# Performance work log

Hardware: AMD Instinct MI355X
Metric: run time of the kernel (lower is better)

The kernel has to match this reference:

```python
import jax, jax.numpy as jnp
import numpy as np

EMB = 128
EDGE = 32
STEPS = 3


def _lrelu(x):
    return jax.nn.leaky_relu(x, negative_slope=0.01)


def setup_inputs() -> dict:
    key = jax.random.key(0)
    ks = jax.random.split(key, 16)
    N, E, G = 50000, 400000, 256
    x = jax.random.normal(ks[0], (N, EMB), jnp.float32)
    edge_attr = jax.random.normal(ks[1], (E, EDGE), jnp.float32)
    edge_index = jax.random.randint(ks[2], (2, E), 0, N, jnp.int64)
    batch_ind = jnp.sort(jax.random.randint(ks[3], (N,), 0, G, jnp.int64))
    data_lens = jax.random.randint(ks[4], (G,), 0, G, jnp.int64)
    s = 1.0 / np.sqrt(EMB)
    Wm = jax.random.normal(ks[5], (STEPS, EMB + EDGE, EMB), jnp.float32) * s
    bm = jnp.zeros((STEPS, EMB), jnp.float32)
    Wa = jax.random.normal(ks[6], (STEPS, 3 * EMB, EMB), jnp.float32) * s
    ba = jnp.zeros((STEPS, EMB), jnp.float32)
    Wgate = jax.random.normal(ks[7], (STEPS, EMB), jnp.float32) * s
    bgate = jnp.zeros((STEPS,), jnp.float32)
    Wfeat = jax.random.normal(ks[8], (STEPS, EMB, EMB), jnp.float32) * s
    bfeat = jnp.zeros((STEPS, EMB), jnp.float32)
    Wt = jax.random.normal(ks[9], (STEPS, 2 * EMB, EMB), jnp.float32) * s
    bt = jnp.zeros((STEPS, EMB), jnp.float32)
    return {"x": x, "edge_attr": edge_attr, "Wm": Wm, "bm": bm, "Wa": Wa,
            "ba": ba, "Wgate": Wgate, "bgate": bgate, "Wfeat": Wfeat,
            "bfeat": bfeat, "Wt": Wt, "bt": bt, "edge_index": edge_index,
            "batch_ind": batch_ind, "num_graphs": 256, "data_lens": data_lens}


def reference(x, edge_attr, Wm, bm, Wa, ba, Wgate, bgate, Wfeat, bfeat, Wt, bt,
              edge_index, batch_ind, num_graphs, data_lens):
    N = x.shape[0]
    src, dst = edge_index[0], edge_index[1]  # PyG: x_j = x[src], aggregate at dst
    xg = jnp.zeros((num_graphs, EMB), x.dtype)  # xg_init is None -> zeros
    for s in range(STEPS):
        # GraphNet: gather -> message MLP -> scatter-max -> update MLP + residual
        xg_node = xg[batch_ind]                                   # [N, emb]
        z = jnp.concatenate([x[src], edge_attr], axis=1)          # [E, emb+edge]
        m = _lrelu(z @ Wm[s] + bm[s])                             # [E, emb]
        agg = jax.ops.segment_max(m, dst, num_segments=N)         # [N, emb]
        agg = jnp.where(jnp.isneginf(agg), 0.0, agg)              # PyG fills empty with 0
        z2 = jnp.concatenate([x, xg_node, agg], axis=1)           # [N, 3*emb]
        x = _lrelu(z2 @ Wa[s] + ba[s]) + x
        # GlobalNode: segment-softmax attention pooling + transform + residual
        gate = x @ Wgate[s] + bgate[s]                            # [N]
        gmax = jax.ops.segment_max(gate, batch_ind, num_segments=num_graphs)
        gmax = jnp.where(jnp.isneginf(gmax), 0.0, gmax)
        e = jnp.exp(gate - gmax[batch_ind])
        denom = jax.ops.segment_sum(e, batch_ind, num_segments=num_graphs)
        alpha = e / denom[batch_ind]                              # [N]
        feat = _lrelu(x @ Wfeat[s] + bfeat[s])                    # [N, emb]
        pooled = jax.ops.segment_sum(alpha[:, None] * feat, batch_ind,
                                     num_segments=num_graphs)     # [G, emb]
        cat = jnp.concatenate([pooled, xg], axis=1)               # [G, 2*emb]
        xg = _lrelu(cat @ Wt[s] + bt[s]) + xg
    return x, xg
```

## Files before the change

kernel.cpp:

```cpp
#include <hip/hip_runtime.h>
#include <hip/hip_bf16.h>

#define EMB 128
#define EDGE 32
#define STEPS 3

typedef short bf8s __attribute__((ext_vector_type(8)));
typedef float f32x4 __attribute__((ext_vector_type(4)));

__device__ __forceinline__ float lrelu(float v) { return v > 0.0f ? v : 0.01f * v; }
__device__ __forceinline__ unsigned short f2bf(float f) {
    unsigned u = __float_as_uint(f);
    u += 0x7fffu + ((u >> 16) & 1u);
    return (unsigned short)(u >> 16);
}
__device__ __forceinline__ float bf2f(unsigned short s) {
    return __uint_as_float(((unsigned)s) << 16);
}
__device__ __forceinline__ unsigned pk2bf(float x, float y) {
    __hip_bfloat162 h = __float22bfloat162_rn(make_float2(x, y));
    return *(unsigned*)&h;
}

__global__ void k_hist(const int* __restrict__ dst, int E, int* __restrict__ deg) {
    int e = blockIdx.x * 256 + threadIdx.x;
    if (e < E) atomicAdd(&deg[dst[e]], 1);
}

__global__ void k_scan1(const int* __restrict__ deg, int N, int* __restrict__ rowptr,
                        int* __restrict__ bsums) {
    __shared__ int s[256];
    int t = threadIdx.x;
    int i = blockIdx.x * 256 + t;
    int v = (i < N) ? deg[i] : 0;
    s[t] = v;
    __syncthreads();
#pragma unroll
    for (int off = 1; off < 256; off <<= 1) {
        int x = (t >= off) ? s[t - off] : 0;
        __syncthreads();
        s[t] += x;
        __syncthreads();
    }
    if (i < N) rowptr[i] = s[t] - v;
    if (t == 255) bsums[blockIdx.x] = s[255];
}

__global__ void k_scan2(int* __restrict__ bsums, int NB) {
    __shared__ int s[256];
    __shared__ int carry;
    int t = threadIdx.x;
    if (t == 0) carry = 0;
    __syncthreads();
    for (int base = 0; base < NB; base += 256) {
        int i = base + t;
        int v = (i < NB) ? bsums[i] : 0;
        s[t] = v;
        __syncthreads();
#pragma unroll
        for (int off = 1; off < 256; off <<= 1) {
            int x = (t >= off) ? s[t - off] : 0;
            __syncthreads();
            s[t] += x;
            __syncthreads();
        }
        int excl = s[t] - v + carry;
        if (i < NB) bsums[i] = excl;
        int tot = s[255];
        __syncthreads();
        if (t == 0) carry += tot;
        __syncthreads();
    }
}

__global__ void k_scan3(int* __restrict__ rowptr, const int* __restrict__ bsums,
                        int* __restrict__ cursor, int N, int E) {
    int i = blockIdx.x * 256 + threadIdx.x;
    if (i < N) {
        int v = rowptr[i] + bsums[i >> 8];
        rowptr[i] = v;
        cursor[i] = v;
    }
    if (i == 0) rowptr[N] = E;
}

__global__ void k_fill(const int* __restrict__ src, const int* __restrict__ dst, int E,
                       int* __restrict__ cursor, int2* __restrict__ sp2) {
    int e = blockIdx.x * 256 + threadIdx.x;
    if (e >= E) return;
    int d = dst[e];
    int p = atomicAdd(&cursor[d], 1);
    sp2[p] = make_int2(src[e], e);
}

__global__ __launch_bounds__(256) void k_eaperm(const float* __restrict__ ea,
                                                const int2* __restrict__ sp2,
                                                unsigned short* __restrict__ ea16p,
                                                int* __restrict__ srcp, int E) {
    int p = blockIdx.x * 256 + threadIdx.x;
    if (p >= E) return;
    int2 sp = sp2[p];
    srcp[p] = sp.x;
    const float4* er = (const float4*)(ea + (size_t)sp.y * EDGE);
    union { unsigned u[16]; int4 v[4]; } o;
#pragma unroll
    for (int q = 0; q < 8; ++q) {
        float4 v = er[q];
        o.u[2 * q]     = pk2bf(v.x, v.y);
        o.u[2 * q + 1] = pk2bf(v.z, v.w);
    }
    int4* dp = (int4*)(ea16p + (size_t)p * EDGE);
#pragma unroll
    for (int q = 0; q < 4; ++q) dp[q] = o.v[q];
}

__global__ __launch_bounds__(256) void k_setup(const float* __restrict__ x0,
                                               unsigned short* __restrict__ x16,
                                               int N, int XB, int NB,
                                               const float* __restrict__ ba,
                                               float* __restrict__ gb,
                                               float* __restrict__ xg_a,
                                               const int* __restrict__ batch,
                                               int* __restrict__ gstart, int G,
                                               unsigned short* __restrict__ h16,
                                               int* __restrict__ deg) {
    int b = blockIdx.x, t = threadIdx.x;
    if (b < XB) {
        size_t idx = ((size_t)b * 256 + t) * 8;
        if (idx < (size_t)N * EMB) {
            const float4* s = (const float4*)(x0 + idx);
            float4 v0 = s[0], v1 = s[1];
            union { bf8s v; unsigned u[4]; } o;
            o.u[0] = pk2bf(v0.x, v0.y);
            o.u[1] = pk2bf(v0.z, v0.w);
            o.u[2] = pk2bf(v1.x, v1.y);
            o.u[3] = pk2bf(v1.z, v1.w);
            *(bf8s*)(x16 + idx) = o.v;
        }
        return;
    }
    b -= XB;
    if (b < NB) {
        int i = b * 256 + t;
        if (i < N) deg[i] = 0;
        return;
    }
    b -= NB;
    if (b < G) {
        if (t < EMB) gb[(size_t)b * EMB + t] = ba[t];
        else xg_a[(size_t)b * EMB + (t - EMB)] = 0.f;
        if (t == 0) {
            int lo = 0, hi = N;
            while (lo < hi) {
                int mid = (lo + hi) >> 1;
                if (batch[mid] < b) lo = mid + 1; else hi = mid;
            }
            gstart[b] = lo;
        }
        return;
    }
    if (t < EMB) h16[(size_t)N * EMB + t] = 0xFF80u;
    if (t == EMB) gstart[G] = N;
}

__global__ __launch_bounds__(256) void k_wpack(const float* __restrict__ Wm,
                                               const float* __restrict__ Wa,
                                               const float* __restrict__ Wfeat,
                                               unsigned short* __restrict__ wpack) {
    int gid = blockIdx.x * 256 + threadIdx.x;
    int unit = gid >> 14;
    int e = gid & 16383;
    int s = unit / 5, u = unit % 5;
    const float* src; int rows;
    switch (u) {
        case 0: src = Wm + (size_t)s * 160 * EMB;             rows = 128; break;
        case 1: src = Wm + (size_t)s * 160 * EMB + 128 * EMB; rows = 32;  break;
        case 2: src = Wa + (size_t)s * 384 * EMB;             rows = 128; break;
        case 3: src = Wa + (size_t)s * 384 * EMB + 256 * EMB; rows = 128; break;
        default: src = Wfeat + (size_t)s * EMB * EMB;         rows = 128; break;
    }
    int k = e >> 7, n = e & 127;
    if (k >= rows) return;
    unsigned short b = f2bf(src[(size_t)k * EMB + n]);
    int kc = k >> 5, c = n >> 4, lane = (n & 15) | (((k & 31) >> 3) << 4), j = k & 7;
    wpack[(size_t)unit * 16384 + ((size_t)(kc * 8 + c) * 64 + lane) * 8 + j] = b;
}

__device__ __forceinline__ void loadAa(const unsigned short* __restrict__ A16, int row0,
                                       int wv, int lane, int N, bf8s af[4]) {
    int li = lane & 15, oct = lane >> 4;
    int m = row0 + wv * 16 + li;
    if (m >= N) m = N - 1;
    const bf8s* ar = (const bf8s*)(A16 + (size_t)m * EMB);
#pragma unroll
    for (int kc = 0; kc < 4; ++kc) af[kc] = ar[kc * 4 + oct];
}
__device__ __forceinline__ void stageB(const unsigned short* __restrict__ Bp,
                                       unsigned short* lB, int tid) {
#pragma unroll
    for (int i = 0; i < 8; ++i) {
        int idx = tid + i * 256;
        ((int4*)lB)[idx] = ((const int4*)Bp)[idx];
    }
}
__device__ __forceinline__ void mfma128r(const bf8s af[4], const unsigned short* lB,
                                         f32x4 acc[8], int lane) {
#pragma unroll
    for (int kc = 0; kc < 4; ++kc) {
#pragma unroll
        for (int c = 0; c < 8; ++c) {
            bf8s b = *(const bf8s*)&lB[((kc * 8 + c) * 64 + lane) * 8];
            acc[c] = __builtin_amdgcn_mfma_f32_16x16x32_bf16(af[kc], b, acc[c], 0, 0, 0);
        }
    }
}

__global__ __launch_bounds__(256) void k_gemm_bias(const unsigned short* __restrict__ A16,
                                                   const unsigned short* __restrict__ Bp,
                                                   const float* __restrict__ bias,
                                                   unsigned short* __restrict__ C, int N) {
    __shared__ unsigned short lB[16384];
    int tid = threadIdx.x, wv = tid >> 6, lane = tid & 63;
    int row0 = blockIdx.x * 64;
    stageB(Bp, lB, tid);
    bf8s af[4];
    loadAa(A16, row0, wv, lane, N, af);
    __syncthreads();
    f32x4 acc[8];
#pragma unroll
    for (int c = 0; c < 8; ++c) acc[c] = (f32x4){0.f, 0.f, 0.f, 0.f};
    mfma128r(af, lB, acc, lane);
    int li = lane & 15, quad = lane >> 4;
    float bcol[8];
#pragma unroll
    for (int c = 0; c < 8; ++c) bcol[c] = bias[c * 16 + li];
#pragma unroll
    for (int rr = 0; rr < 4; ++rr) {
        int m = row0 + wv * 16 + quad * 4 + rr;
        if (m < N) {
            union { bf8s v; unsigned u[4]; } o;
#pragma unroll
            for (int j = 0; j < 4; ++j)
                o.u[j] = pk2bf(acc[2 * j][rr] + bcol[2 * j],
                               acc[2 * j + 1][rr] + bcol[2 * j + 1]);
            *(bf8s*)&C[(size_t)m * EMB + li * 8] = o.v;
        }
    }
}

__global__ __launch_bounds__(256) void k_gemm_node(unsigned short* __restrict__ x16,
                                                   const unsigned short* __restrict__ agg16,
                                                   const unsigned short* __restrict__ BpX,
                                                   const unsigned short* __restrict__ BpA,
                                                   const float* __restrict__ gb,
                                                   const int* __restrict__ batch,
                                                   float* __restrict__ xout_f32,
                                                   const float* __restrict__ wg,
                                                   const float* __restrict__ bg,
                                                   float* __restrict__ gate, int N) {
    __shared__ unsigned short lB[16384];
    int tid = threadIdx.x, wv = tid >> 6, lane = tid & 63;
    int row0 = blockIdx.x * 64;
    stageB(BpX, lB, tid);
    bf8s af[4];
    loadAa(x16, row0, wv, lane, N, af);
    __syncthreads();
    f32x4 acc[8];
#pragma unroll
    for (int c = 0; c < 8; ++c) acc[c] = (f32x4){0.f, 0.f, 0.f, 0.f};
    mfma128r(af, lB, acc, lane);
    __syncthreads();
    stageB(BpA, lB, tid);
    loadAa(agg16, row0, wv, lane, N, af);
    __syncthreads();
    mfma128r(af, lB, acc, lane);
    int li = lane & 15, quad = lane >> 4;
    float gpart[4] = {0.f, 0.f, 0.f, 0.f};
#pragma unroll
    for (int c = 0; c < 8; ++c) {
        int col = c * 16 + li;
        float wgc = wg[col];
#pragma unroll
        for (int rr = 0; rr < 4; ++rr) {
            int m = row0 + wv * 16 + quad * 4 + rr;
            if (m < N) {
                int g = batch[m];
                float b = gb[(size_t)g * EMB + col];
                float res = bf2f(x16[(size_t)m * EMB + col]);
                float v = lrelu(acc[c][rr] + b) + res;
                x16[(size_t)m * EMB + col] = f2bf(v);
                if (xout_f32) xout_f32[(size_t)m * EMB + col] = v;
                gpart[rr] = fmaf(v, wgc, gpart[rr]);
            }
        }
    }
#pragma unroll
    for (int rr = 0; rr < 4; ++rr) {
#pragma unroll
        for (int off = 1; off < 16; off <<= 1)
            gpart[rr] += __shfl_xor(gpart[rr], off, 64);
    }
    if (li == 0) {
        float b0 = bg[0];
#pragma unroll
        for (int rr = 0; rr < 4; ++rr) {
            int m = row0 + wv * 16 + quad * 4 + rr;
            if (m < N) gate[m] = gpart[rr] + b0;
        }
    }
}

__global__ __launch_bounds__(256) void k_gemm_feat(const unsigned short* __restrict__ A16,
                                                   const unsigned short* __restrict__ Bp,
                                                   const float* __restrict__ bias,
                                                   const float* __restrict__ gate,
                                                   const float* __restrict__ gmax,
                                                   const float* __restrict__ denom,
                                                   const int* __restrict__ batch,
                                                   float* __restrict__ pooled, int N) {
    __shared__ unsigned short lB[16384];
    int tid = threadIdx.x, wv = tid >> 6, lane = tid & 63;
    int row0 = blockIdx.x * 64;
    stageB(Bp, lB, tid);
    bf8s af[4];
    loadAa(A16, row0, wv, lane, N, af);
    __syncthreads();
    f32x4 acc[8];
#pragma unroll
    for (int c = 0; c < 8; ++c) acc[c] = (f32x4){0.f, 0.f, 0.f, 0.f};
    mfma128r(af, lB, acc, lane);
    int li = lane & 15, quad = lane >> 4;
    int rb = row0 + wv * 16;
    if (rb >= N) return;
    float alpha[4];
    int grow[4];
#pragma unroll
    for (int rr = 0; rr < 4; ++rr) {
        int m = rb + quad * 4 + rr;
        if (m < N) {
            int g = batch[m];
            grow[rr] = g;
            alpha[rr] = __expf(gate[m] - gmax[g]) / denom[g];
        } else { alpha[rr] = 0.f; grow[rr] = 0; }
    }
    int gs = batch[rb];
    int mlast = rb + 15; if (mlast >= N) mlast = N - 1;
    bool uni = (gs == batch[mlast]);
#pragma unroll
    for (int c = 0; c < 8; ++c) {
        int col = c * 16 + li;
        float b = bias[col];
        float v0 = alpha[0] * lrelu(acc[c][0] + b);
        float v1 = alpha[1] * lrelu(acc[c][1] + b);
        float v2 = alpha[2] * lrelu(acc[c][2] + b);
        float v3 = alpha[3] * lrelu(acc[c][3] + b);
        if (uni) {
            float s = (v0 + v1) + (v2 + v3);
            s += __shfl_xor(s, 16, 64);
            s += __shfl_xor(s, 32, 64);
            if (quad == 0) atomicAdd(&pooled[(size_t)gs * EMB + col], s);
        } else {
            if (rb + quad * 4 + 0 < N) atomicAdd(&pooled[(size_t)grow[0] * EMB + col], v0);
            if (rb + quad * 4 + 1 < N) atomicAdd(&pooled[(size_t)grow[1] * EMB + col], v1);
            if (rb + quad * 4 + 2 < N) atomicAdd(&pooled[(size_t)grow[2] * EMB + col], v2);
            if (rb + quad * 4 + 3 < N) atomicAdd(&pooled[(size_t)grow[3] * EMB + col], v3);
        }
    }
}

__global__ __launch_bounds__(256) void k_gseg(const float* __restrict__ gate,
                                              const int* __restrict__ gstart,
                                              float* __restrict__ gmax,
                                              float* __restrict__ denom,
                                              float* __restrict__ pooled) {
    int g = blockIdx.x;
    int t = threadIdx.x;
    if (t < EMB) pooled[(size_t)g * EMB + t] = 0.f;
    int s0 = gstart[g], s1 = gstart[g + 1];
    __shared__ float red[256];
    float mx = -__builtin_inff();
    for (int i = s0 + t; i < s1; i += 256) mx = fmaxf(mx, gate[i]);
    red[t] = mx;
    __syncthreads();
#pragma unroll
    for (int off = 128; off; off >>= 1) {
        if (t < off) red[t] = fmaxf(red[t], red[t + off]);
        __syncthreads();
    }
    float m = red[0];
    __syncthreads();
    float sum = 0.f;
    for (int i = s0 + t; i < s1; i += 256) sum += __expf(gate[i] - m);
    red[t] = sum;
    __syncthreads();
#pragma unroll
    for (int off = 128; off; off >>= 1) {
        if (t < off) red[t] += red[t + off];
        __syncthreads();
    }
    if (t == 0) {
        gmax[g] = (s1 > s0) ? m : 0.f;
        denom[g] = red[0];
    }
}

__global__ __launch_bounds__(128) void k_xg(const float* __restrict__ pooled,
                                            const float* __restrict__ xg,
                                            const float* __restrict__ Wt,
                                            const float* __restrict__ bt,
                                            float* __restrict__ xg_out,
                                            const float* __restrict__ WaGn,
                                            const float* __restrict__ ban,
                                            float* __restrict__ gb) {
    int g = blockIdx.x, c = threadIdx.x;
    __shared__ float row[256];
    row[c] = pooled[(size_t)g * EMB + c];
    row[c + 128] = xg[(size_t)g * EMB + c];
    __syncthreads();
    float acc = bt[c];
#pragma unroll 8
    for (int k = 0; k < 256; ++k) acc = fmaf(row[k], Wt[(size_t)k * EMB + c], acc);
    float v = lrelu(acc) + row[c + 128];
    xg_out[(size_t)g * EMB + c] = v;
    if (WaGn) {
        __syncthreads();
        row[c] = v;
        __syncthreads();
        float a2 = ban[c];
#pragma unroll 8
        for (int k = 0; k < EMB; ++k) a2 = fmaf(row[k], WaGn[(size_t)k * EMB + c], a2);
        gb[(size_t)g * EMB + c] = a2;
    }
}

__global__ __launch_bounds__(256) void k_fagg(const unsigned short* __restrict__ h,
                                              const unsigned short* __restrict__ ea16p,
                                              const int* __restrict__ srcp,
                                              const int* __restrict__ rowptr,
                                              const unsigned short* __restrict__ Bp,
                                              unsigned short* __restrict__ agg, int N) {
    __shared__ unsigned short lB[4096];
    int tid = threadIdx.x;
    ((int4*)lB)[tid]       = ((const int4*)Bp)[tid];
    ((int4*)lB)[tid + 256] = ((const int4*)Bp)[tid + 256];
    __syncthreads();
    int wv = tid >> 6, lane = tid & 63;
    int li = lane & 15, oct = lane >> 4;
    int nA = blockIdx.x * 8 + wv * 2;
    if (nA >= N) return;
    int nB = nA + 1;
    bool hasB = (nB < N);
    int r0 = rowptr[nA];
    int r1 = rowptr[nA + 1];
    int r2 = hasB ? rowptr[nB + 1] : r1;
    int degA = r1 - r0, degB = r2 - r1;

    float vmA[8], vmB[8];
#pragma unroll
    for (int ci = 0; ci < 8; ++ci) { vmA[ci] = -__builtin_inff(); vmB[ci] = -__builtin_inff(); }

    {
        int pA = r0 + li; if (pA >= r1) pA = (r1 > r0) ? r1 - 1 : 0;
        int pB = r1 + li; if (pB >= r2) pB = (r2 > r1) ? r2 - 1 : 0;
        int srcvA = srcp[pA];
        int srcvB = srcp[pB];
        bf8s aA = *(const bf8s*)&ea16p[(size_t)pA * EDGE + oct * 8];
        bf8s aB = *(const bf8s*)&ea16p[(size_t)pB * EDGE + oct * 8];
        union { bf8s v; unsigned short s[8]; } hvA[4], hvB[4];
#pragma unroll
        for (int rr = 0; rr < 4; ++rr) {
            int sr = __shfl(srcvA, oct * 4 + rr, 16);
            if (oct * 4 + rr >= degA) sr = N;
            hvA[rr].v = *(const bf8s*)&h[(size_t)sr * EMB + li * 8];
        }
#pragma unroll
        for (int rr = 0; rr < 4; ++rr) {
            int sr = __shfl(srcvB, oct * 4 + rr, 16);
            if (oct * 4 + rr >= degB) sr = N;
            hvB[rr].v = *(const bf8s*)&h[(size_t)sr * EMB + li * 8];
        }
#pragma unroll
        for (int ci = 0; ci < 8; ++ci) {
            bf8s bb = *(const bf8s*)&lB[(ci * 64 + lane) * 8];
            f32x4 acc;
            acc[0] = bf2f(hvA[0].s[ci]);
            acc[1] = bf2f(hvA[1].s[ci]);
            acc[2] = bf2f(hvA[2].s[ci]);
            acc[3] = bf2f(hvA[3].s[ci]);
            acc = __builtin_amdgcn_mfma_f32_16x16x32_bf16(aA, bb, acc, 0, 0, 0);
#pragma unroll
            for (int rr = 0; rr < 4; ++rr) vmA[ci] = fmaxf(vmA[ci], acc[rr]);
        }
#pragma unroll
        for (int ci = 0; ci < 8; ++ci) {
            bf8s bb = *(const bf8s*)&lB[(ci * 64 + lane) * 8];
            f32x4 acc;
            acc[0] = bf2f(hvB[0].s[ci]);
            acc[1] = bf2f(hvB[1].s[ci]);
            acc[2] = bf2f(hvB[2].s[ci]);
            acc[3] = bf2f(hvB[3].s[ci]);
            acc = __builtin_amdgcn_mfma_f32_16x16x32_bf16(aB, bb, acc, 0, 0, 0);
#pragma unroll
            for (int rr = 0; rr < 4; ++rr) vmB[ci] = fmaxf(vmB[ci], acc[rr]);
        }
    }
    for (int b = 16; b < degA; b += 16) {
        int p = r0 + b + li;
        if (p > r1 - 1) p = r1 - 1;
        int srcv = srcp[p];
        bf8s a = *(const bf8s*)&ea16p[(size_t)p * EDGE + oct * 8];
        union { bf8s v; unsigned short s[8]; } hv[4];
#pragma unroll
        for (int rr = 0; rr < 4; ++rr) {
            int sr = __shfl(srcv, oct * 4 + rr, 16);
            if (b + oct * 4 + rr >= degA) sr = N;
            hv[rr].v = *(const bf8s*)&h[(size_t)sr * EMB + li * 8];
        }
#pragma unroll
        for (int ci = 0; ci < 8; ++ci) {
            bf8s bb = *(const bf8s*)&lB[(ci * 64 + lane) * 8];
            f32x4 acc;
            acc[0] = bf2f(hv[0].s[ci]);
            acc[1] = bf2f(hv[1].s[ci]);
            acc[2] = bf2f(hv[2].s[ci]);
            acc[3] = bf2f(hv[3].s[ci]);
            acc = __builtin_amdgcn_mfma_f32_16x16x32_bf16(a, bb, acc, 0, 0, 0);
#pragma unroll
            for (int rr = 0; rr < 4; ++rr) vmA[ci] = fmaxf(vmA[ci], acc[rr]);
        }
    }
    for (int b = 16; b < degB; b += 16) {
        int p = r1 + b + li;
        if (p > r2 - 1) p = r2 - 1;
        int srcv = srcp[p];
        bf8s a = *(const bf8s*)&ea16p[(size_t)p * EDGE + oct * 8];
        union { bf8s v; unsigned short s[8]; } hv[4];
#pragma unroll
        for (int rr = 0; rr < 4; ++rr) {
            int sr = __shfl(srcv, oct * 4 + rr, 16);
            if (b + oct * 4 + rr >= degB) sr = N;
            hv[rr].v = *(const bf8s*)&h[(size_t)sr * EMB + li * 8];
        }
#pragma unroll
        for (int ci = 0; ci < 8; ++ci) {
            bf8s bb = *(const bf8s*)&lB[(ci * 64 + lane) * 8];
            f32x4 acc;
            acc[0] = bf2f(hv[0].s[ci]);
            acc[1] = bf2f(hv[1].s[ci]);
            acc[2] = bf2f(hv[2].s[ci]);
            acc[3] = bf2f(hv[3].s[ci]);
            acc = __builtin_amdgcn_mfma_f32_16x16x32_bf16(a, bb, acc, 0, 0, 0);
#pragma unroll
            for (int rr = 0; rr < 4; ++rr) vmB[ci] = fmaxf(vmB[ci], acc[rr]);
        }
    }
#pragma unroll
    for (int ci = 0; ci < 8; ++ci) {
        vmA[ci] = fmaxf(vmA[ci], __shfl_xor(vmA[ci], 16, 64));
        vmA[ci] = fmaxf(vmA[ci], __shfl_xor(vmA[ci], 32, 64));
        vmB[ci] = fmaxf(vmB[ci], __shfl_xor(vmB[ci], 16, 64));
        vmB[ci] = fmaxf(vmB[ci], __shfl_xor(vmB[ci], 32, 64));
    }
    {
        float s0 = (oct == 0) ? vmA[0] : (oct == 1) ? vmA[1] : (oct == 2) ? vmA[2] : vmA[3];
        float s1 = (oct == 0) ? vmA[4] : (oct == 1) ? vmA[5] : (oct == 2) ? vmA[6] : vmA[7];
        s0 = lrelu(s0);
        s1 = lrelu(s1);
        if (degA == 0) { s0 = 0.f; s1 = 0.f; }
        agg[(size_t)nA * EMB + oct * 16 + li]       = f2bf(s0);
        agg[(size_t)nA * EMB + (oct + 4) * 16 + li] = f2bf(s1);
    }
    if (hasB) {
        float s0 = (oct == 0) ? vmB[0] : (oct == 1) ? vmB[1] : (oct == 2) ? vmB[2] : vmB[3];
        float s1 = (oct == 0) ? vmB[4] : (oct == 1) ? vmB[5] : (oct == 2) ? vmB[6] : vmB[7];
        s0 = lrelu(s0);
        s1 = lrelu(s1);
        if (degB == 0) { s0 = 0.f; s1 = 0.f; }
        agg[(size_t)nB * EMB + oct * 16 + li]       = f2bf(s0);
        agg[(size_t)nB * EMB + (oct + 4) * 16 + li] = f2bf(s1);
    }
}

extern "C" void kernel_launch(void* const* d_in, const int* in_sizes, int n_in,
                              void* d_out, int out_size, void* d_ws, size_t ws_size,
                              hipStream_t stream) {
    const float* x0    = (const float*)d_in[0];
    const float* ea    = (const float*)d_in[1];
    const float* Wm    = (const float*)d_in[2];
    const float* bm    = (const float*)d_in[3];
    const float* Wa    = (const float*)d_in[4];
    const float* ba    = (const float*)d_in[5];
    const float* Wgate = (const float*)d_in[6];
    const float* bgate = (const float*)d_in[7];
    const float* Wfeat = (const float*)d_in[8];
    const float* bfeat = (const float*)d_in[9];
    const float* Wt    = (const float*)d_in[10];
    const float* bt    = (const float*)d_in[11];
    const int*   eidx  = (const int*)d_in[12];
    const int*   batch = (const int*)d_in[13];

    int N = in_sizes[0] / EMB;
    int E = in_sizes[1] / EDGE;
    int G = in_sizes[15];

    char* w = (char*)d_ws;
    auto alloc = [&](size_t bytes) {
        char* p = w;
        w += (bytes + 255) & ~(size_t)255;
        return p;
    };
    unsigned short* h16   = (unsigned short*)alloc((size_t)(N + 1) * EMB * 2);
    unsigned short* x16   = (unsigned short*)alloc((size_t)N * EMB * 2);
    unsigned short* agg16 = (unsigned short*)alloc((size_t)N * EMB * 2);
    float* gate   = (float*)alloc((size_t)N * 4);
    float* gb     = (float*)alloc((size_t)G * EMB * 4);
    float* pooled = (float*)alloc((size_t)G * EMB * 4);
    float* gmax   = (float*)alloc((size_t)G * 4);
    float* denom  = (float*)alloc((size_t)G * 4);
    float* xg_a   = (float*)alloc((size_t)G * EMB * 4);
    float* xg_b   = (float*)alloc((size_t)G * EMB * 4);
    int* deg      = (int*)alloc((size_t)N * 4);
    int* rowptr   = (int*)alloc((size_t)(N + 1) * 4);
    int* cursor   = (int*)alloc((size_t)N * 4);
    int2* sp2     = (int2*)alloc((size_t)E * 8);
    int* srcp     = (int*)alloc((size_t)E * 4);
    unsigned short* ea16p = (unsigned short*)alloc((size_t)E * EDGE * 2);
    int* gstart   = (int*)alloc((size_t)(G + 1) * 4);
    int* bsums    = (int*)alloc(1024 * 4);
    unsigned short* wpack = (unsigned short*)alloc((size_t)15 * 16384 * 2);

    const int* esrc = eidx;
    const int* edst = eidx + E;
    int ebl = (E + 255) / 256;
    int NB  = (N + 255) / 256;
    int XB  = ((size_t)N * EMB / 8 + 255) / 256;

    k_setup<<<XB + NB + G + 1, 256, 0, stream>>>(x0, x16, N, XB, NB, ba, gb, xg_a,
                                                 batch, gstart, G, h16, deg);
    k_hist<<<ebl, 256, 0, stream>>>(edst, E, deg);
    k_scan1<<<NB, 256, 0, stream>>>(deg, N, rowptr, bsums);
    k_scan2<<<1, 256, 0, stream>>>(bsums, NB);
    k_scan3<<<NB, 256, 0, stream>>>(rowptr, bsums, cursor, N, E);
    k_fill<<<ebl, 256, 0, stream>>>(esrc, edst, E, cursor, sp2);
    k_eaperm<<<ebl, 256, 0, stream>>>(ea, sp2, ea16p, srcp, E);
    k_wpack<<<960, 256, 0, stream>>>(Wm, Wa, Wfeat, wpack);

    int gemm_blocks = (N + 63) / 64;
    int fagg_blocks = (N + 7) / 8;

    float* xg_cur = xg_a;
    float* xg_nxt = xg_b;

    for (int s = 0; s < STEPS; ++s) {
        const unsigned short* wp = wpack + (size_t)s * 5 * 16384;
        bool last = (s == STEPS - 1);

        k_gemm_bias<<<gemm_blocks, 256, 0, stream>>>(x16, wp + 0 * 16384, bm + s * EMB,
                                                     h16, N);
        k_fagg<<<fagg_blocks, 256, 0, stream>>>(h16, ea16p, srcp, rowptr, wp + 1 * 16384,
                                                agg16, N);
        k_gemm_node<<<gemm_blocks, 256, 0, stream>>>(x16, agg16, wp + 2 * 16384,
                                                     wp + 3 * 16384, gb, batch,
                                                     last ? (float*)d_out : nullptr,
                                                     Wgate + s * EMB, bgate + s, gate, N);
        k_gseg<<<G, 256, 0, stream>>>(gate, gstart, gmax, denom, pooled);
        k_gemm_feat<<<gemm_blocks, 256, 0, stream>>>(x16, wp + 4 * 16384, bfeat + s * EMB,
                                                     gate, gmax, denom, batch, pooled, N);
        const float* WaGn = !last ? Wa + (size_t)(s + 1) * 384 * EMB + 128 * EMB : nullptr;
        const float* ban  = !last ? ba + (s + 1) * EMB : nullptr;
        float* xgout = last ? (float*)d_out + (size_t)N * EMB : xg_nxt;
        k_xg<<<G, 128, 0, stream>>>(pooled, xg_cur, Wt + (size_t)s * 256 * EMB,
                                    bt + s * EMB, xgout, WaGn, ban, gb);

        float* tmp = xg_cur; xg_cur = xg_nxt; xg_nxt = tmp;
    }
}
```

Measured before the change: 530.7 us.

## Fuse next step's message GEMM into the feature-pooling GEMM kernel

The per-step message-projection GEMM (x @ Wm + bm) is removed from the loop head. It is computed once before the loop for step 0, and for later steps inside a new combined kernel that also does the feature GEMM and pooling. The combined kernel reuses the A-fragments of x already loaded in registers and restages the LDS B tile with the next step's weights. This saves one launch and one read of x per step, but doubles the accumulator registers, which may lower occupancy, and adds extra syncs for the restaging.

```diff
diff --git a/kernel.cpp b/kernel.cpp
--- a/kernel.cpp
+++ b/kernel.cpp
@@ -215,6 +215,27 @@
     }
 }
 
+__device__ __forceinline__ void bias_epi(const f32x4 acc[8], int row0, int wv, int lane,
+                                         const float* __restrict__ bias,
+                                         unsigned short* __restrict__ C, int N) {
+    int li = lane & 15, quad = lane >> 4;
+    float bcol[8];
+#pragma unroll
+    for (int c = 0; c < 8; ++c) bcol[c] = bias[c * 16 + li];
+#pragma unroll
+    for (int rr = 0; rr < 4; ++rr) {
+        int m = row0 + wv * 16 + quad * 4 + rr;
+        if (m < N) {
+            union { bf8s v; unsigned u[4]; } o;
+#pragma unroll
+            for (int j = 0; j < 4; ++j)
+                o.u[j] = pk2bf(acc[2 * j][rr] + bcol[2 * j],
+                               acc[2 * j + 1][rr] + bcol[2 * j + 1]);
+            *(bf8s*)&C[(size_t)m * EMB + li * 8] = o.v;
+        }
+    }
+}
+
 __global__ __launch_bounds__(256) void k_gemm_bias(const unsigned short* __restrict__ A16,
                                                    const unsigned short* __restrict__ Bp,
                                                    const float* __restrict__ bias,
@@ -230,22 +251,7 @@
 #pragma unroll
     for (int c = 0; c < 8; ++c) acc[c] = (f32x4){0.f, 0.f, 0.f, 0.f};
     mfma128r(af, lB, acc, lane);
-    int li = lane & 15, quad = lane >> 4;
-    float bcol[8];
-#pragma unroll
-    for (int c = 0; c < 8; ++c) bcol[c] = bias[c * 16 + li];
-#pragma unroll
-    for (int rr = 0; rr < 4; ++rr) {
-        int m = row0 + wv * 16 + quad * 4 + rr;
-        if (m < N) {
-            union { bf8s v; unsigned u[4]; } o;
-#pragma unroll
-            for (int j = 0; j < 4; ++j)
-                o.u[j] = pk2bf(acc[2 * j][rr] + bcol[2 * j],
-                               acc[2 * j + 1][rr] + bcol[2 * j + 1]);
-            *(bf8s*)&C[(size_t)m * EMB + li * 8] = o.v;
-        }
-    }
+    bias_epi(acc, row0, wv, lane, bias, C, N);
 }
 
 __global__ __launch_bounds__(256) void k_gemm_node(unsigned short* __restrict__ x16,
@@ -310,25 +316,13 @@
     }
 }
 
-__global__ __launch_bounds__(256) void k_gemm_feat(const unsigned short* __restrict__ A16,
-                                                   const unsigned short* __restrict__ Bp,
-                                                   const float* __restrict__ bias,
-                                                   const float* __restrict__ gate,
-                                                   const float* __restrict__ gmax,
-                                                   const float* __restrict__ denom,
-                                                   const int* __restrict__ batch,
-                                                   float* __restrict__ pooled, int N) {
-    __shared__ unsigned short lB[16384];
-    int tid = threadIdx.x, wv = tid >> 6, lane = tid & 63;
-    int row0 = blockIdx.x * 64;
-    stageB(Bp, lB, tid);
-    bf8s af[4];
-    loadAa(A16, row0, wv, lane, N, af);
-    __syncthreads();
-    f32x4 acc[8];
-#pragma unroll
-    for (int c = 0; c < 8; ++c) acc[c] = (f32x4){0.f, 0.f, 0.f, 0.f};
-    mfma128r(af, lB, acc, lane);
+__device__ __forceinline__ void feat_epi(const f32x4 acc[8], int row0, int wv, int lane,
+                                         const float* __restrict__ bias,
+                                         const float* __restrict__ gate,
+                                         const float* __restrict__ gmax,
+                                         const float* __restrict__ denom,
+                                         const int* __restrict__ batch,
+                                         float* __restrict__ pooled, int N) {
     int li = lane & 15, quad = lane >> 4;
     int rb = row0 + wv * 16;
     if (rb >= N) return;
@@ -366,6 +360,61 @@
             if (rb + quad * 4 + 3 < N) atomicAdd(&pooled[(size_t)grow[3] * EMB + col], v3);
         }
     }
+}
+
+__global__ __launch_bounds__(256) void k_gemm_feat(const unsigned short* __restrict__ A16,
+                                                   const unsigned short* __restrict__ Bp,
+                                                   const float* __restrict__ bias,
+                                                   const float* __restrict__ gate,
+                                                   const float* __restrict__ gmax,
+                                                   const float* __restrict__ denom,
+                                                   const int* __restrict__ batch,
+                                                   float* __restrict__ pooled, int N) {
+    __shared__ unsigned short lB[16384];
+    int tid = threadIdx.x, wv = tid >> 6, lane = tid & 63;
+    int row0 = blockIdx.x * 64;
+    stageB(Bp, lB, tid);
+    bf8s af[4];
+    loadAa(A16, row0, wv, lane, N, af);
+    __syncthreads();
+    f32x4 acc[8];
+#pragma unroll
+    for (int c = 0; c < 8; ++c) acc[c] = (f32x4){0.f, 0.f, 0.f, 0.f};
+    mfma128r(af, lB, acc, lane);
+    feat_epi(acc, row0, wv, lane, bias, gate, gmax, denom, batch, pooled, N);
+}
+
+__global__ __launch_bounds__(256) void k_gemm_fb(const unsigned short* __restrict__ A16,
+                                                 const unsigned short* __restrict__ BpF,
+                                                 const float* __restrict__ bfeat_s,
+                                                 const float* __restrict__ gate,
+                                                 const float* __restrict__ gmax,
+                                                 const float* __restrict__ denom,
+                                                 const int* __restrict__ batch,
+                                                 float* __restrict__ pooled,
+                                                 const unsigned short* __restrict__ BpBn,
+                                                 const float* __restrict__ bm_next,
+                                                 unsigned short* __restrict__ h16, int N) {
+    __shared__ unsigned short lB[16384];
+    int tid = threadIdx.x, wv = tid >> 6, lane = tid & 63;
+    int row0 = blockIdx.x * 64;
+    stageB(BpF, lB, tid);
+    bf8s af[4];
+    loadAa(A16, row0, wv, lane, N, af);
+    __syncthreads();
+    f32x4 accF[8], accB[8];
+#pragma unroll
+    for (int c = 0; c < 8; ++c) {
+        accF[c] = (f32x4){0.f, 0.f, 0.f, 0.f};
+        accB[c] = (f32x4){0.f, 0.f, 0.f, 0.f};
+    }
+    mfma128r(af, lB, accF, lane);
+    __syncthreads();
+    stageB(BpBn, lB, tid);
+    __syncthreads();
+    mfma128r(af, lB, accB, lane);
+    feat_epi(accF, row0, wv, lane, bfeat_s, gate, gmax, denom, batch, pooled, N);
+    bias_epi(accB, row0, wv, lane, bm_next, h16, N);
 }
 
 __global__ __launch_bounds__(256) void k_gseg(const float* __restrict__ gate,
@@ -651,12 +700,12 @@
     float* xg_cur = xg_a;
     float* xg_nxt = xg_b;
 
+    k_gemm_bias<<<gemm_blocks, 256, 0, stream>>>(x16, wpack + 0 * 16384, bm, h16, N);
+
     for (int s = 0; s < STEPS; ++s) {
         const unsigned short* wp = wpack + (size_t)s * 5 * 16384;
         bool last = (s == STEPS - 1);
 
-        k_gemm_bias<<<gemm_blocks, 256, 0, stream>>>(x16, wp + 0 * 16384, bm + s * EMB,
-                                                     h16, N);
         k_fagg<<<fagg_blocks, 256, 0, stream>>>(h16, ea16p, srcp, rowptr, wp + 1 * 16384,
                                                 agg16, N);
         k_gemm_node<<<gemm_blocks, 256, 0, stream>>>(x16, agg16, wp + 2 * 16384,
@@ -664,8 +713,16 @@
                                                      last ? (float*)d_out : nullptr,
                                                      Wgate + s * EMB, bgate + s, gate, N);
         k_gseg<<<G, 256, 0, stream>>>(gate, gstart, gmax, denom, pooled);
-        k_gemm_feat<<<gemm_blocks, 256, 0, stream>>>(x16, wp + 4 * 16384, bfeat + s * EMB,
-                                                     gate, gmax, denom, batch, pooled, N);
+        if (!last) {
+            k_gemm_fb<<<gemm_blocks, 256, 0, stream>>>(x16, wp + 4 * 16384, bfeat + s * EMB,
+                                                       gate, gmax, denom, batch, pooled,
+                                                       wp + 5 * 16384 ,
+                                                       bm + (s + 1) * EMB, h16, N);
+        } else {
+            k_gemm_feat<<<gemm_blocks, 256, 0, stream>>>(x16, wp + 4 * 16384,
+                                                         bfeat + s * EMB, gate, gmax,
+                                                         denom, batch, pooled, N);
+        }
         const float* WaGn = !last ? Wa + (size_t)(s + 1) * 384 * EMB + 128 * EMB : nullptr;
         const float* ban  = !last ? ba + (s + 1) * EMB : nullptr;
         float* xgout = last ? (float*)d_out + (size_t)N * EMB : xg_nxt;
```

After: 518.4 us. 2.3% less time.
